# Optimization experiments

Measured on AMD Instinct MI355X. Metric: run time of the kernel, lower is better.

## Reference

```python
import jax, jax.numpy as jnp
import numpy as np

B, T, N, F, C, H, O = 4, 8, 4096, 32, 32, 64, 1
RADIUS = 50.0   # adjacency_threshold on pairwise distance
EPS = 1e-5      # batchnorm eps


def setup_inputs() -> dict:
    key = jax.random.key(0)
    ks = jax.random.split(key, 8)
    x = jax.random.normal(ks[0], (B, T, N, F), jnp.float32)
    # dist_mat from random 2D node locations in a 1000x1000 area; avg degree ~32
    loc = jax.random.uniform(ks[1], (N, 2), jnp.float32) * 1000.0
    d2 = jnp.sum((loc[:, None, :] - loc[None, :, :]) ** 2, axis=-1)  # [N,N]
    adj = (d2 < RADIUS ** 2).astype(jnp.float32)                     # includes self (d=0)
    dinv = 1.0 / jnp.sqrt(jnp.maximum(adj.sum(-1), 1.0))
    adj_norm = adj * dinv[:, None] * dinv[None, :]                   # D^-1/2 A D^-1/2
    s = 0.05
    return dict(
        x=x,
        adj_norm=adj_norm,
        bn_gamma=jnp.ones((F,), jnp.float32),
        bn_beta=jnp.zeros((F,), jnp.float32),
        W_gcn=jax.random.normal(ks[2], (F, C), jnp.float32) * s,
        b_gcn=jnp.zeros((C,), jnp.float32),
        W_ih=jax.random.normal(ks[3], (C, 3 * H), jnp.float32) * s,
        W_hh=jax.random.normal(ks[4], (H, 3 * H), jnp.float32) * s,
        b_ih=jnp.zeros((3 * H,), jnp.float32),
        b_hh=jnp.zeros((3 * H,), jnp.float32),
        W_dense=jax.random.normal(ks[5], (H, O), jnp.float32) * s,
        b_dense=jnp.zeros((O,), jnp.float32),
    )


def reference(x, adj_norm, bn_gamma, bn_beta, W_gcn, b_gcn, W_ih, W_hh, b_ih, b_hh, W_dense, b_dense):
    # BatchNorm2d over feature channel (training-mode batch stats, biased var)
    mean = x.mean(axis=(0, 1, 2))
    var = x.var(axis=(0, 1, 2))
    xn = (x - mean) * jax.lax.rsqrt(var + EPS) * bn_gamma + bn_beta  # [B,T,N,F]
    # GCN association (same math every timestep -> batch over T)
    ya = jnp.einsum('mn,btnf->btmf', adj_norm, xn)                   # neighbor aggregate
    y = jnp.einsum('btnf,fc->btnc', ya, W_gcn) + b_gcn               # [B,T,N,C]
    # precompute input-gate projections, then scan GRU cell over time
    gi = jnp.einsum('btnc,ch->btnh', y, W_ih) + b_ih                 # [B,T,N,3H]
    gi = jnp.transpose(gi, (1, 0, 2, 3))                             # [T,B,N,3H]

    def step(h, g):
        gh = h @ W_hh + b_hh
        r = jax.nn.sigmoid(g[..., :H] + gh[..., :H])
        z = jax.nn.sigmoid(g[..., H:2 * H] + gh[..., H:2 * H])
        n = jnp.tanh(g[..., 2 * H:] + r * gh[..., 2 * H:])
        h_new = (1.0 - z) * n + z * h
        return h_new, h_new

    h0 = jnp.zeros((B, N, H), x.dtype)
    _, hs = jax.lax.scan(step, h0, gi)                               # [T,B,N,H]
    out = jnp.transpose(hs, (1, 0, 2, 3)) @ W_dense + b_dense        # [B,T,N,O]
    return out
```

## Files before the change

kernel.cpp:

```cpp
#include <hip/hip_runtime.h>
#include <hip/hip_bf16.h>
#include <stdint.h>

#define B_ 4
#define T_ 8
#define N_ 4096
#define F_ 32
#define BT_ (B_*T_)
#define ROWS_ (B_*N_)
#define CAP_ 128
#define EPS_ 1e-5f
#define NELEM_ (B_*T_*N_*F_)

#define WS_BNP    0
#define WS_ROWSUM 16384
#define WS_DEG    (WS_ROWSUM + 4096)
#define WS_FRG    (WS_DEG + 4096)
#define WS_PAIR   (WS_FRG + 52*256)
#define WS_XA     (WS_PAIR + 4096*CAP_*2)

typedef float v4f __attribute__((ext_vector_type(4)));
typedef _Float16 half8 __attribute__((ext_vector_type(8)));
union HU { uint32_t u[4]; half8 v; };

__device__ inline float sigm_f(float x) {
  return __builtin_amdgcn_rcpf(1.0f + __expf(-x));
}
__device__ inline uint32_t f16pair(float a, float b) {
  union { _Float16 h; unsigned short s; } x, y;
  x.h = (_Float16)a; y.h = (_Float16)b;
  return (uint32_t)x.s | ((uint32_t)y.s << 16);
}
__device__ inline void sp2(float a0, float a1, uint32_t& hi, uint32_t& lo) {
  _Float16 h0 = (_Float16)a0, h1 = (_Float16)a1;
  float r0 = a0 - (float)h0, r1 = a1 - (float)h1;
  union { _Float16 h; unsigned short s; } u0, u1, v0, v1;
  u0.h = h0; u1.h = h1; v0.h = (_Float16)r0; v1.h = (_Float16)r1;
  hi = (uint32_t)u0.s | ((uint32_t)u1.s << 16);
  lo = (uint32_t)v0.s | ((uint32_t)v1.s << 16);
}

__global__ void __launch_bounds__(256)
k_pre(const float* __restrict__ x, const float* __restrict__ A, float* __restrict__ ws) {
  if (blockIdx.x < 2048) {
    int m0 = blockIdx.x * 2;
    __shared__ int cnt[2];
    __shared__ float wsum[4][2];
    if (threadIdx.x < 2) cnt[threadIdx.x] = 0;
    __syncthreads();
    int* deg = (int*)&ws[WS_DEG];
    float2* pair = (float2*)&ws[WS_PAIR];
    const float4* A4 = (const float4*)(A + (size_t)m0 * N_);
    float4 av4[8];
#pragma unroll
    for (int r = 0; r < 2; r++)
#pragma unroll
      for (int i = 0; i < 4; i++) av4[r * 4 + i] = A4[r * 1024 + threadIdx.x + 256 * i];
    float lsum[2] = {0.f, 0.f};
#pragma unroll
    for (int r = 0; r < 2; r++)
#pragma unroll
      for (int i = 0; i < 4; i++) {
        float av[4] = {av4[r*4+i].x, av4[r*4+i].y, av4[r*4+i].z, av4[r*4+i].w};
        int nb4 = (threadIdx.x + 256 * i) * 4;
#pragma unroll
        for (int e = 0; e < 4; e++) {
          float a = av[e];
          if (a != 0.0f) {
            int p = atomicAdd(&cnt[r], 1);
            if (p < CAP_) pair[(size_t)(m0 + r) * CAP_ + p] = make_float2(__int_as_float((nb4 + e) * F_), a);
            lsum[r] += a;
          }
        }
      }
#pragma unroll
    for (int r = 0; r < 2; r++) {
      float s = lsum[r];
#pragma unroll
      for (int off = 32; off > 0; off >>= 1) s += __shfl_xor(s, off, 64);
      if ((threadIdx.x & 63) == 0) wsum[threadIdx.x >> 6][r] = s;
    }
    __syncthreads();
#pragma unroll
    for (int r = 0; r < 2; r++) {
      int c = cnt[r];
      for (int p = c + threadIdx.x; p < 68; p += 256)
        pair[(size_t)(m0 + r) * CAP_ + p] = make_float2(__int_as_float(0), 0.0f);
    }
    if (threadIdx.x < 2) {
      int r = threadIdx.x;
      deg[m0 + r] = min(cnt[r], CAP_);
      ws[WS_ROWSUM + m0 + r] = wsum[0][r] + wsum[1][r] + wsum[2][r] + wsum[3][r];
    }
  } else {
    int bnb = blockIdx.x - 2048;
    const float4* x4 = (const float4*)x;
    int tid = bnb * 256 + threadIdx.x;
    float s[4] = {0,0,0,0}, s2[4] = {0,0,0,0};
    for (int i = tid; i < NELEM_ / 4; i += 256 * 256) {
      float4 v = x4[i];
      s[0] += v.x; s2[0] += v.x * v.x;
      s[1] += v.y; s2[1] += v.y * v.y;
      s[2] += v.z; s2[2] += v.z * v.z;
      s[3] += v.w; s2[3] += v.w * v.w;
    }
    __shared__ float ls[256][4], ls2[256][4];
#pragma unroll
    for (int r = 0; r < 4; r++) { ls[threadIdx.x][r] = s[r]; ls2[threadIdx.x][r] = s2[r]; }
    __syncthreads();
    int t = threadIdx.x;
    if (t < 32) {
      int g = t >> 2, r = t & 3;
      float a = 0.f;
      for (int q = g; q < 256; q += 8) a += ls[q][r];
      ws[WS_BNP + bnb * 64 + t] = a;
    } else if (t < 64) {
      int cch = t - 32;
      int g = cch >> 2, r = cch & 3;
      float b2 = 0.f;
      for (int q = g; q < 256; q += 8) b2 += ls2[q][r];
      ws[WS_BNP + bnb * 64 + t] = b2;
    }
  }
}

__global__ void __launch_bounds__(256)
k_fold(const float* __restrict__ gamma, const float* __restrict__ beta,
       const float* __restrict__ Wg, const float* __restrict__ bg,
       const float* __restrict__ Wih, const float* __restrict__ bih,
       const float* __restrict__ Whh, const float* __restrict__ bhh,
       float* __restrict__ ws) {
  __shared__ float fb[26144];
  __shared__ float bnp4[4][64];
  float* Wx_s  = fb;
  float* Wih_s = fb + 6144;
  float* Whh_s = fb + 12288;
  float* Wg_s  = fb + 24576;
  float* Us_s  = fb + 25600;
  float* Vs_s  = fb + 25792;
  float* bns   = fb + 25984;
  float* scale_s = fb + 26048;
  float* shift_s = fb + 26080;
  float* p_s   = fb + 26112;
  int tid = threadIdx.x;
#pragma unroll
  for (int i = tid; i < 1536; i += 256) ((float4*)Wih_s)[i] = ((const float4*)Wih)[i];
#pragma unroll
  for (int i = tid; i < 3072; i += 256) ((float4*)Whh_s)[i] = ((const float4*)Whh)[i];
  if (tid < 256) { ((float4*)Wg_s)[tid] = ((const float4*)Wg)[tid]; }
  {
    int g = tid >> 6, c = tid & 63;
    float a = 0.f;
    for (int i = 0; i < 64; i++) a += ws[WS_BNP + (size_t)(g + 4 * i) * 64 + c];
    bnp4[g][c] = a;
  }
  __syncthreads();
  if (tid < 64) bns[tid] = bnp4[0][tid] + bnp4[1][tid] + bnp4[2][tid] + bnp4[3][tid];
  __syncthreads();
  if (tid < 32) {
    float cntf = (float)(B_ * T_ * N_);
    float mean = bns[tid] / cntf;
    float var = bns[32 + tid] / cntf - mean * mean;
    float sc = gamma[tid] * rsqrtf(var + EPS_);
    scale_s[tid] = sc;
    shift_s[tid] = beta[tid] - mean * sc;
  }
  __syncthreads();
  if (tid < 32) {
    float acc = 0.f;
    for (int f = 0; f < 32; f++) acc += shift_s[f] * Wg_s[f * 32 + tid];
    p_s[tid] = acc;
  }
  __syncthreads();
  for (int e = tid; e < 32 * 192; e += 256) {
    int f = e / 192, j = e % 192;
    float acc = 0.f;
#pragma unroll
    for (int c = 0; c < 32; c++) acc += Wg_s[f * 32 + c] * Wih_s[c * 192 + j];
    Wx_s[e] = scale_s[f] * acc;
  }
  if (tid < 192) {
    float au = 0.f, av = 0.f;
#pragma unroll
    for (int c = 0; c < 32; c++) { au += p_s[c] * Wih_s[c * 192 + tid]; av += bg[c] * Wih_s[c * 192 + tid]; }
    Us_s[tid] = au; Vs_s[tid] = av + bih[tid];
  }
  __syncthreads();
  int w = tid >> 6, L = tid & 63, q = L >> 4, c = L & 15;
  uint32_t* wsu = (uint32_t*)ws;
  for (int fi = w; fi < 52; fi += 4) {
    int mt, kt;
    if (fi < 32)      { mt = fi >> 2;            kt = fi & 3; }
    else if (fi < 40) { mt = 8 + ((fi - 32) >> 1); kt = (fi & 1) ? 3 : 0; }
    else              { int r = fi - 40; mt = 12 + r / 3; kt = 1 + r % 3; }
    int cls = mt >> 2;
    int col = (cls < 2) ? mt * 16 + c : 128 + (mt & 3) * 16 + c;
#pragma unroll
    for (int d = 0; d < 4; d++) {
      float a01[2];
#pragma unroll
      for (int h2 = 0; h2 < 2; h2++) {
        int k = kt * 32 + q * 8 + 2 * d + h2;
        float v;
        if (k < 32)       v = (cls == 3) ? 0.f : Wx_s[k * 192 + col];
        else if (k < 96)  v = (cls == 2) ? 0.f : Whh_s[(k - 32) * 192 + col];
        else if (k == 96) v = (cls == 3) ? 0.f : Us_s[col];
        else if (k == 97) v = (cls < 2) ? (Vs_s[col] + bhh[col]) : (cls == 2 ? Vs_s[col] : bhh[col]);
        else              v = 0.f;
        a01[h2] = v;
      }
      wsu[WS_FRG + fi * 256 + L * 4 + d] = f16pair(a01[0], a01[1]);
    }
  }
}

#define AGG_STEP(d) { \
    float vv = pv[d]; \
    v4f t0 = pb0[d], t1 = pb1[d]; \
    float2 p = pl[row * 69 + k + 4 + d]; \
    int off = __float_as_int(p.x) + fo; \
    pv[d] = p.y; \
    pb0[d] = *(const v4f*)(xb0 + off); \
    pb1[d] = *(const v4f*)(xb1 + off); \
    acc0 += vv * t0; acc1 += vv * t1; }

__global__ void __launch_bounds__(256, 8)
k_agg(const float* __restrict__ x, float* __restrict__ ws) {
  __shared__ float2 pl[32 * 69];
  int tid = threadIdx.x;
  int chunk = blockIdx.x & 15;
  int mg = blockIdx.x >> 4;
  int row = tid >> 3, f4 = tid & 7;
  int m = mg * 32 + row;
  const int* deg = (const int*)&ws[WS_DEG];
  const float2* pair = (const float2*)&ws[WS_PAIR];
  for (int qq = tid; qq < 32 * 68; qq += 256) {
    int r = qq / 68, sl = qq - r * 68;
    pl[r * 69 + sl] = pair[(size_t)(mg * 32 + r) * CAP_ + sl];
  }
  __syncthreads();
  int d0 = deg[m];
  int dm = min(d0, 64);
  int bound = dm;
  bound = max(bound, __shfl_xor(bound, 8, 64));
  bound = max(bound, __shfl_xor(bound, 16, 64));
  bound = max(bound, __shfl_xor(bound, 32, 64));
  bound = (bound + 3) & ~3;
  int bt0 = chunk * 2;
  const float* xb0 = x + (size_t)bt0 * N_ * F_;
  const float* xb1 = xb0 + N_ * F_;
  int fo = f4 * 4;
  v4f acc0 = {0,0,0,0}, acc1 = {0,0,0,0};
  v4f pb0[4], pb1[4];
  float pv[4];
#pragma unroll
  for (int d = 0; d < 4; d++) {
    float2 p = pl[row * 69 + d];
    int off = __float_as_int(p.x) + fo;
    pv[d] = p.y;
    pb0[d] = *(const v4f*)(xb0 + off);
    pb1[d] = *(const v4f*)(xb1 + off);
  }
  for (int k = 0; k < bound; k += 4) {
    AGG_STEP(0) AGG_STEP(1) AGG_STEP(2) AGG_STEP(3)
  }
  if (d0 > 64) {
    for (int k = 64; k < d0; k++) {
      float2 p = pair[(size_t)m * CAP_ + k];
      int off = __float_as_int(p.x) + fo;
      float vv = p.y;
      acc0 += vv * *(const v4f*)(xb0 + off);
      acc1 += vv * *(const v4f*)(xb1 + off);
    }
  }
  size_t ob = (size_t)bt0 * N_ * F_ + m * F_ + fo;
  *(v4f*)(ws + WS_XA + ob) = acc0;
  *(v4f*)(ws + WS_XA + ob + (size_t)N_ * F_) = acc1;
}

#define LDA(fi) (*(const half8*)(frg + (fi)*256 + L*4))
#define DO1(A_, fi, BH, BL) { half8 af = LDA(fi); \
  A_ = __builtin_amdgcn_mfma_f32_16x16x32_f16(af, BH, A_, 0, 0, 0); \
  A_ = __builtin_amdgcn_mfma_f32_16x16x32_f16(af, BL, A_, 0, 0, 0); }
#define DO1C(A_, C_, fi, BH, BL) { half8 af = LDA(fi); \
  A_ = __builtin_amdgcn_mfma_f32_16x16x32_f16(af, BH, C_, 0, 0, 0); \
  A_ = __builtin_amdgcn_mfma_f32_16x16x32_f16(af, BL, A_, 0, 0, 0); }

__global__ void __launch_bounds__(256, 2)
k_gru(const float* __restrict__ Wd, const float* __restrict__ bd,
      const float* __restrict__ ws, float* __restrict__ out) {
  __shared__ uint32_t frg[52 * 256];
  __shared__ uint32_t hx[2 * 1344];
  __shared__ float obuf[2][16];
  {
    const uint4* gf = (const uint4*)(ws + WS_FRG);
    uint4* sf = (uint4*)frg;
    for (int i = threadIdx.x; i < 52 * 64; i += 256) sf[i] = gf[i];
  }
  __syncthreads();
  int wid = threadIdx.x >> 6, L = threadIdx.x & 63;
  int grp = wid >> 1, half = wid & 1, h2 = half * 2;
  int q = L >> 4, c = L & 15;
  uint32_t* hxg = hx + grp * 1344;
  int rg0 = blockIdx.x * 32 + grp * 16;
  int b = rg0 >> 12;
  int node0 = rg0 & (N_ - 1);
  int fR0 = 4 * h2, fR1 = 4 * h2 + 4;
  int fZ0 = 16 + 4 * h2, fZ1 = 20 + 4 * h2;
  int fN0 = 32 + 2 * h2, fN1 = 34 + 2 * h2;
  int fG0 = 40 + 3 * h2, fG1 = 43 + 3 * h2;
  float wdv[2][4];
#pragma unroll
  for (int lg = 0; lg < 2; lg++)
#pragma unroll
    for (int r = 0; r < 4; r++) wdv[lg][r] = Wd[16 * (h2 + lg) + 4 * q + r];
  float bdv = bd[0];

  HU b3h, b3l;
#pragma unroll
  for (int d = 0; d < 4; d++) { b3h.u[d] = 0; b3l.u[d] = 0; }
  {
    float rsv = ws[WS_ROWSUM + node0 + c];
    uint32_t rhi, rlo;
    sp2(rsv, 1.0f, rhi, rlo);
    if (q == 0) { b3h.u[0] = rhi; b3l.u[0] = rlo & 0xFFFFu; }
  }

  v4f bias[8];
  {
    v4f z4 = {0.f, 0.f, 0.f, 0.f};
    DO1C(bias[0], z4, fR0 + 3, b3h.v, b3l.v)
    DO1C(bias[1], z4, fR1 + 3, b3h.v, b3l.v)
    DO1C(bias[2], z4, fZ0 + 3, b3h.v, b3l.v)
    DO1C(bias[3], z4, fZ1 + 3, b3h.v, b3l.v)
    DO1C(bias[4], z4, fN0 + 1, b3h.v, b3l.v)
    DO1C(bias[5], z4, fN1 + 1, b3h.v, b3l.v)
    DO1C(bias[6], z4, fG0 + 2, b3h.v, b3l.v)
    DO1C(bias[7], z4, fG1 + 2, b3h.v, b3l.v)
  }

  float h[2][4];
#pragma unroll
  for (int lg = 0; lg < 2; lg++)
#pragma unroll
    for (int r = 0; r < 4; r++) h[lg][r] = 0.f;

  const float* xab = ws + WS_XA;
  size_t xo0 = ((size_t)(b * T_) * N_ + node0 + c) * F_ + q * 8;
  float4 curA = *(const float4*)(xab + xo0);
  float4 curB = *(const float4*)(xab + xo0 + 4);
  float4 nxA, nxB;

#pragma unroll 1
  for (int t = 0; t < T_; t++) {
    HU b1h, b1l, b2h, b2l;
    if (t > 0) {
#pragma unroll
      for (int d = 0; d < 4; d++) {
        b1h.u[d] = hxg[((4 * q + d) * 2 + 0) * 21 + c];
        b1l.u[d] = hxg[((4 * q + d) * 2 + 1) * 21 + c];
        b2h.u[d] = hxg[((16 + 4 * q + d) * 2 + 0) * 21 + c];
        b2l.u[d] = hxg[((16 + 4 * q + d) * 2 + 1) * 21 + c];
      }
    }
    __syncthreads();
    if (t < T_ - 1) {
      size_t xo = ((size_t)(b * T_ + t + 1) * N_ + node0 + c) * F_ + q * 8;
      nxA = *(const float4*)(xab + xo);
      nxB = *(const float4*)(xab + xo + 4);
    }
    HU b0h, b0l;
    sp2(curA.x, curA.y, b0h.u[0], b0l.u[0]);
    sp2(curA.z, curA.w, b0h.u[1], b0l.u[1]);
    sp2(curB.x, curB.y, b0h.u[2], b0l.u[2]);
    sp2(curB.z, curB.w, b0h.u[3], b0l.u[3]);
    v4f acc[8];
    if (t > 0) {
      DO1C(acc[0], bias[0], fR0 + 1, b1h.v, b1l.v)
      DO1C(acc[1], bias[1], fR1 + 1, b1h.v, b1l.v)
      DO1C(acc[2], bias[2], fZ0 + 1, b1h.v, b1l.v)
      DO1C(acc[3], bias[3], fZ1 + 1, b1h.v, b1l.v)
      DO1C(acc[6], bias[6], fG0,     b1h.v, b1l.v)
      DO1C(acc[7], bias[7], fG1,     b1h.v, b1l.v)
      DO1(acc[0], fR0 + 2, b2h.v, b2l.v)
      DO1(acc[1], fR1 + 2, b2h.v, b2l.v)
      DO1(acc[2], fZ0 + 2, b2h.v, b2l.v)
      DO1(acc[3], fZ1 + 2, b2h.v, b2l.v)
      DO1(acc[6], fG0 + 1, b2h.v, b2l.v)
      DO1(acc[7], fG1 + 1, b2h.v, b2l.v)
      DO1(acc[0], fR0, b0h.v, b0l.v)
      DO1(acc[1], fR1, b0h.v, b0l.v)
      DO1(acc[2], fZ0, b0h.v, b0l.v)
      DO1(acc[3], fZ1, b0h.v, b0l.v)
      DO1C(acc[4], bias[4], fN0, b0h.v, b0l.v)
      DO1C(acc[5], bias[5], fN1, b0h.v, b0l.v)
    } else {
      DO1C(acc[0], bias[0], fR0, b0h.v, b0l.v)
      DO1C(acc[1], bias[1], fR1, b0h.v, b0l.v)
      DO1C(acc[2], bias[2], fZ0, b0h.v, b0l.v)
      DO1C(acc[3], bias[3], fZ1, b0h.v, b0l.v)
      DO1C(acc[4], bias[4], fN0, b0h.v, b0l.v)
      DO1C(acc[5], bias[5], fN1, b0h.v, b0l.v)
      acc[6] = bias[6]; acc[7] = bias[7];
    }
    float o = 0.f;
#pragma unroll
    for (int lg = 0; lg < 2; lg++)
#pragma unroll
      for (int r = 0; r < 4; r++) {
        float rr = sigm_f(acc[lg][r]);
        float zz = sigm_f(acc[2 + lg][r]);
        float nn = 2.0f * sigm_f(2.0f * (acc[4 + lg][r] + rr * acc[6 + lg][r])) - 1.0f;
        float hn = zz * (h[lg][r] - nn) + nn;
        h[lg][r] = hn;
        o += wdv[lg][r] * hn;
      }
    o += __shfl_xor(o, 16, 64);
    o += __shfl_xor(o, 32, 64);
    if (half == 1 && L < 16) obuf[grp][L] = o;
    if (t < T_ - 1) {
#pragma unroll
      for (int lg = 0; lg < 2; lg++)
#pragma unroll
        for (int rp = 0; rp < 2; rp++) {
          uint32_t phi, plo;
          sp2(h[lg][2 * rp], h[lg][2 * rp + 1], phi, plo);
          int pidx = 8 * (h2 + lg) + 2 * q + rp;
          hxg[(pidx * 2 + 0) * 21 + c] = phi;
          hxg[(pidx * 2 + 1) * 21 + c] = plo;
        }
    }
    __syncthreads();
    if (half == 0 && L < 16)
      out[(size_t)(b * T_ + t) * N_ + node0 + L] = o + obuf[grp][L] + bdv;
    curA = nxA; curB = nxB;
  }
}

extern "C" void kernel_launch(void* const* d_in, const int* in_sizes, int n_in,
                              void* d_out, int out_size, void* d_ws, size_t ws_size,
                              hipStream_t stream) {
  const float* x     = (const float*)d_in[0];
  const float* adj   = (const float*)d_in[1];
  const float* gamma = (const float*)d_in[2];
  const float* beta  = (const float*)d_in[3];
  const float* Wg    = (const float*)d_in[4];
  const float* bg    = (const float*)d_in[5];
  const float* Wih   = (const float*)d_in[6];
  const float* Whh   = (const float*)d_in[7];
  const float* bih   = (const float*)d_in[8];
  const float* bhh   = (const float*)d_in[9];
  const float* Wd    = (const float*)d_in[10];
  const float* bd    = (const float*)d_in[11];
  float* ws = (float*)d_ws;
  float* out = (float*)d_out;

  k_pre<<<2048 + 256, 256, 0, stream>>>(x, adj, ws);
  k_fold<<<1, 256, 0, stream>>>(gamma, beta, Wg, bg, Wih, bih, Whh, bhh, ws);
  k_agg<<<2048, 256, 0, stream>>>(x, ws);
  k_gru<<<512, 256, 0, stream>>>(Wd, bd, ws, out);
}
```

Before: 203.4 us.

## Fold weight-prep kernel into aggregation launch as 52 parallel fragment blocks

Removes the single-block k_fold launch and merges its work into the aggregation kernel, giving each of the 52 fp16 weight fragments its own block that computes only the columns it needs. This removes one kernel launch and the serial tail of a one-block kernel, and spreads the weight folding across many CUs. The cost is that BN statistics are now recomputed redundantly in many blocks. It also relies on k_gru being the only consumer of the fragments, since the aggregation blocks and fragment blocks run concurrently.

```diff
diff --git a/kernel.cpp b/kernel.cpp
--- a/kernel.cpp
+++ b/kernel.cpp
@@ -124,96 +124,6 @@
   }
 }
 
-__global__ void __launch_bounds__(256)
-k_fold(const float* __restrict__ gamma, const float* __restrict__ beta,
-       const float* __restrict__ Wg, const float* __restrict__ bg,
-       const float* __restrict__ Wih, const float* __restrict__ bih,
-       const float* __restrict__ Whh, const float* __restrict__ bhh,
-       float* __restrict__ ws) {
-  __shared__ float fb[26144];
-  __shared__ float bnp4[4][64];
-  float* Wx_s  = fb;
-  float* Wih_s = fb + 6144;
-  float* Whh_s = fb + 12288;
-  float* Wg_s  = fb + 24576;
-  float* Us_s  = fb + 25600;
-  float* Vs_s  = fb + 25792;
-  float* bns   = fb + 25984;
-  float* scale_s = fb + 26048;
-  float* shift_s = fb + 26080;
-  float* p_s   = fb + 26112;
-  int tid = threadIdx.x;
-#pragma unroll
-  for (int i = tid; i < 1536; i += 256) ((float4*)Wih_s)[i] = ((const float4*)Wih)[i];
-#pragma unroll
-  for (int i = tid; i < 3072; i += 256) ((float4*)Whh_s)[i] = ((const float4*)Whh)[i];
-  if (tid < 256) { ((float4*)Wg_s)[tid] = ((const float4*)Wg)[tid]; }
-  {
-    int g = tid >> 6, c = tid & 63;
-    float a = 0.f;
-    for (int i = 0; i < 64; i++) a += ws[WS_BNP + (size_t)(g + 4 * i) * 64 + c];
-    bnp4[g][c] = a;
-  }
-  __syncthreads();
-  if (tid < 64) bns[tid] = bnp4[0][tid] + bnp4[1][tid] + bnp4[2][tid] + bnp4[3][tid];
-  __syncthreads();
-  if (tid < 32) {
-    float cntf = (float)(B_ * T_ * N_);
-    float mean = bns[tid] / cntf;
-    float var = bns[32 + tid] / cntf - mean * mean;
-    float sc = gamma[tid] * rsqrtf(var + EPS_);
-    scale_s[tid] = sc;
-    shift_s[tid] = beta[tid] - mean * sc;
-  }
-  __syncthreads();
-  if (tid < 32) {
-    float acc = 0.f;
-    for (int f = 0; f < 32; f++) acc += shift_s[f] * Wg_s[f * 32 + tid];
-    p_s[tid] = acc;
-  }
-  __syncthreads();
-  for (int e = tid; e < 32 * 192; e += 256) {
-    int f = e / 192, j = e % 192;
-    float acc = 0.f;
-#pragma unroll
-    for (int c = 0; c < 32; c++) acc += Wg_s[f * 32 + c] * Wih_s[c * 192 + j];
-    Wx_s[e] = scale_s[f] * acc;
-  }
-  if (tid < 192) {
-    float au = 0.f, av = 0.f;
-#pragma unroll
-    for (int c = 0; c < 32; c++) { au += p_s[c] * Wih_s[c * 192 + tid]; av += bg[c] * Wih_s[c * 192 + tid]; }
-    Us_s[tid] = au; Vs_s[tid] = av + bih[tid];
-  }
-  __syncthreads();
-  int w = tid >> 6, L = tid & 63, q = L >> 4, c = L & 15;
-  uint32_t* wsu = (uint32_t*)ws;
-  for (int fi = w; fi < 52; fi += 4) {
-    int mt, kt;
-    if (fi < 32)      { mt = fi >> 2;            kt = fi & 3; }
-    else if (fi < 40) { mt = 8 + ((fi - 32) >> 1); kt = (fi & 1) ? 3 : 0; }
-    else              { int r = fi - 40; mt = 12 + r / 3; kt = 1 + r % 3; }
-    int cls = mt >> 2;
-    int col = (cls < 2) ? mt * 16 + c : 128 + (mt & 3) * 16 + c;
-#pragma unroll
-    for (int d = 0; d < 4; d++) {
-      float a01[2];
-#pragma unroll
-      for (int h2 = 0; h2 < 2; h2++) {
-        int k = kt * 32 + q * 8 + 2 * d + h2;
-        float v;
-        if (k < 32)       v = (cls == 3) ? 0.f : Wx_s[k * 192 + col];
-        else if (k < 96)  v = (cls == 2) ? 0.f : Whh_s[(k - 32) * 192 + col];
-        else if (k == 96) v = (cls == 3) ? 0.f : Us_s[col];
-        else if (k == 97) v = (cls < 2) ? (Vs_s[col] + bhh[col]) : (cls == 2 ? Vs_s[col] : bhh[col]);
-        else              v = 0.f;
-        a01[h2] = v;
-      }
-      wsu[WS_FRG + fi * 256 + L * 4 + d] = f16pair(a01[0], a01[1]);
-    }
-  }
-}
-
 #define AGG_STEP(d) { \
     float vv = pv[d]; \
     v4f t0 = pb0[d], t1 = pb1[d]; \
@@ -225,11 +135,117 @@
     acc0 += vv * t0; acc1 += vv * t1; }
 
 __global__ void __launch_bounds__(256, 8)
-k_agg(const float* __restrict__ x, float* __restrict__ ws) {
+k_aggf(const float* __restrict__ x, const float* __restrict__ gamma,
+       const float* __restrict__ beta, const float* __restrict__ Wg,
+       const float* __restrict__ bg, const float* __restrict__ Wih,
+       const float* __restrict__ bih, const float* __restrict__ Whh,
+       const float* __restrict__ bhh, float* __restrict__ ws) {
   __shared__ float2 pl[32 * 69];
   int tid = threadIdx.x;
-  int chunk = blockIdx.x & 15;
-  int mg = blockIdx.x >> 4;
+  if (blockIdx.x < 52) {
+    float* fs   = (float*)pl;
+    float* bnp4 = fs;
+    float* bns  = fs + 256;
+    float* scl  = fs + 320;
+    float* shf  = fs + 352;
+    float* ps   = fs + 384;
+    float* Wg_s = fs + 416;
+    float* Wic  = fs + 1440;
+    float* Wxc  = fs + 1952;
+    float* UsV  = fs + 2464;
+    float* Whc  = fs + 2496;
+    int fi = blockIdx.x;
+    int mt, kt;
+    if (fi < 32)      { mt = fi >> 2;              kt = fi & 3; }
+    else if (fi < 40) { mt = 8 + ((fi - 32) >> 1); kt = (fi & 1) ? 3 : 0; }
+    else              { int r = fi - 40; mt = 12 + r / 3; kt = 1 + r % 3; }
+    int cls = mt >> 2;
+    int colbase = (cls < 2) ? mt * 16 : 128 + (mt & 3) * 16;
+    if (kt == 1 || kt == 2) {
+      for (int e = tid; e < 512; e += 256) {
+        int r = e >> 4, cc = e & 15;
+        Whc[e] = Whh[(size_t)((kt - 1) * 32 + r) * 192 + colbase + cc];
+      }
+    } else {
+      ((float4*)Wg_s)[tid] = ((const float4*)Wg)[tid];
+      for (int e = tid; e < 512; e += 256) {
+        int r = e >> 4, cc = e & 15;
+        Wic[e] = Wih[(size_t)r * 192 + colbase + cc];
+      }
+      int g = tid >> 6, cch = tid & 63;
+      float a = 0.f;
+      for (int i = 0; i < 64; i++) a += ws[WS_BNP + (size_t)(g + 4 * i) * 64 + cch];
+      bnp4[g * 64 + cch] = a;
+    }
+    __syncthreads();
+    if ((kt == 0 || kt == 3) && tid < 64)
+      bns[tid] = bnp4[tid] + bnp4[64 + tid] + bnp4[128 + tid] + bnp4[192 + tid];
+    __syncthreads();
+    if ((kt == 0 || kt == 3) && tid < 32) {
+      float cntf = (float)(B_ * T_ * N_);
+      float mean = bns[tid] / cntf;
+      float var = bns[32 + tid] / cntf - mean * mean;
+      float sc = gamma[tid] * rsqrtf(var + EPS_);
+      scl[tid] = sc;
+      shf[tid] = beta[tid] - mean * sc;
+    }
+    __syncthreads();
+    if (kt == 3 && tid < 32) {
+      float acc = 0.f;
+#pragma unroll
+      for (int f = 0; f < 32; f++) acc += shf[f] * Wg_s[f * 32 + tid];
+      ps[tid] = acc;
+    }
+    __syncthreads();
+    if (kt == 0) {
+      for (int e = tid; e < 512; e += 256) {
+        int f = e >> 4, cc = e & 15;
+        float acc = 0.f;
+#pragma unroll
+        for (int m = 0; m < 32; m++) acc += Wg_s[f * 32 + m] * Wic[m * 16 + cc];
+        Wxc[e] = scl[f] * acc;
+      }
+    } else if (kt == 3) {
+      if (tid < 16) {
+        float au = 0.f;
+#pragma unroll
+        for (int c2 = 0; c2 < 32; c2++) au += ps[c2] * Wic[c2 * 16 + tid];
+        UsV[tid] = au;
+      } else if (tid < 32) {
+        int cc = tid - 16;
+        float av = 0.f;
+#pragma unroll
+        for (int c2 = 0; c2 < 32; c2++) av += bg[c2] * Wic[c2 * 16 + cc];
+        UsV[16 + cc] = av + bih[colbase + cc];
+      }
+    }
+    __syncthreads();
+    if (tid < 64) {
+      int L = tid, q = L >> 4, c = L & 15;
+      uint32_t* wsu = (uint32_t*)ws;
+#pragma unroll
+      for (int d = 0; d < 4; d++) {
+        float a01[2];
+#pragma unroll
+        for (int h2 = 0; h2 < 2; h2++) {
+          int kk = q * 8 + 2 * d + h2;
+          float v;
+          if (kt == 0)       v = Wxc[kk * 16 + c];
+          else if (kt != 3)  v = Whc[kk * 16 + c];
+          else if (kk == 0)  v = (cls == 3) ? 0.f : UsV[c];
+          else if (kk == 1)  v = (cls < 2) ? (UsV[16 + c] + bhh[colbase + c])
+                                           : (cls == 2 ? UsV[16 + c] : bhh[colbase + c]);
+          else               v = 0.f;
+          a01[h2] = v;
+        }
+        wsu[WS_FRG + fi * 256 + L * 4 + d] = f16pair(a01[0], a01[1]);
+      }
+    }
+    return;
+  }
+  int bid2 = blockIdx.x - 52;
+  int chunk = bid2 & 15;
+  int mg = bid2 >> 4;
   int row = tid >> 3, f4 = tid & 7;
   int m = mg * 32 + row;
   const int* deg = (const int*)&ws[WS_DEG];
@@ -456,7 +472,6 @@
   float* out = (float*)d_out;
 
   k_pre<<<2048 + 256, 256, 0, stream>>>(x, adj, ws);
-  k_fold<<<1, 256, 0, stream>>>(gamma, beta, Wg, bg, Wih, bih, Whh, bhh, ws);
-  k_agg<<<2048, 256, 0, stream>>>(x, ws);
+  k_aggf<<<52 + 2048, 256, 0, stream>>>(x, gamma, beta, Wg, bg, Wih, bih, Whh, bhh, ws);
   k_gru<<<512, 256, 0, stream>>>(Wd, bd, ws, out);
 }
```

Measured after the change: 199.1 us. 2.1% less time.
